# Optimization experiments

Measured on AMD Instinct MI355X. Metric: run time of the kernel, lower is better.

The kernel has to match this reference:

```python
import jax, jax.numpy as jnp
import numpy as np

B, N, F_IN, F_OUT, H = 2, 4096, 256, 64, 4


def setup_inputs() -> dict:
    key = jax.random.key(0)
    k_adj, k_h, k_w, k_l, k_r = jax.random.split(key, 5)
    adj = jax.random.randint(k_adj, (B, N, N), 0, 2, dtype=jnp.int32)
    h = jax.random.normal(k_h, (B, N, F_IN), dtype=jnp.float32)
    # xavier-uniform-ish params
    lim_w = float(np.sqrt(6.0 / (F_IN + F_OUT)))
    W = jax.random.uniform(k_w, (F_IN, F_OUT), jnp.float32, -lim_w, lim_w)
    lim_a = float(np.sqrt(6.0 / (F_OUT + H)))
    Wl = jax.random.uniform(k_l, (H, F_OUT), jnp.float32, -lim_a, lim_a)  # attn_l.weight
    Wr = jax.random.uniform(k_r, (H, F_OUT), jnp.float32, -lim_a, lim_a)  # attn_r.weight
    b = jnp.zeros((F_OUT,), jnp.float32)
    return {"adj": adj, "h": h, "W": W, "Wl": Wl, "Wr": Wr, "b": b}


def reference(adj, h, W, Wl, Wr, b):
    # dropout layers are identity in eval mode
    x = jnp.einsum('bnf,fo->bno', h, W)                       # (B,N,F_OUT)
    el = jnp.einsum('bno,ho->bnh', x, Wl)                     # (B,N,H)
    er = jnp.einsum('bno,ho->bnh', x, Wr)                     # (B,N,H)
    attn = el[:, :, None, :] + er[:, None, :, :]              # (B,N,N,H)
    attn = jax.nn.leaky_relu(attn, negative_slope=0.2)
    attn = jnp.where(adj[..., None] == 0, -jnp.inf, attn)
    attn = jax.nn.softmax(attn, axis=2)                       # softmax over source nodes j
    out = jnp.einsum('bijh,bjf->bihf', attn, x)               # (B,N,H,F_OUT)
    out = out + b                                             # bias over feature dim
    out = jax.nn.elu(out)                                     # activation
    return out.reshape(B, N, H * F_OUT)                       # n_heads>1 concat; B>1 keeps batch
```

## Files before the change

### kernel.cpp

```cpp
#include <hip/hip_runtime.h>
#include <hip/hip_bf16.h>


#define NN 4096
#define NH 4
#define JT 64
#define IT 64
#define NSET 4
#define NJQ 4
#define NTS ((NN / NJQ) / JT)
#define LOG2E 1.4426950408889634f

typedef __bf16 bf16x8 __attribute__((ext_vector_type(8)));
typedef unsigned short ushortx8 __attribute__((ext_vector_type(8)));
typedef unsigned short us4 __attribute__((ext_vector_type(4)));
typedef float f32x4 __attribute__((ext_vector_type(4)));

__device__ __forceinline__ void gload_lds16(const void* g, void* lds) {
  __builtin_amdgcn_global_load_lds(
      (const __attribute__((address_space(1))) void*)g,
      (__attribute__((address_space(3))) void*)lds, 16, 0, 0);
}

__device__ __forceinline__ unsigned short f2bf(float x) {
  __hip_bfloat16 hb = __float2bfloat16(x);
  return __builtin_bit_cast(unsigned short, hb);
}

#if __has_builtin(__builtin_amdgcn_exp2f)
#define EXP2F(x) __builtin_amdgcn_exp2f(x)
#else
#define EXP2F(x) exp2f(x)
#endif

__global__ __launch_bounds__(256, 2) void gat_prep(
    const float* __restrict__ hmat, const float* __restrict__ W,
    const float* __restrict__ Wl, const float* __restrict__ Wr,
    unsigned short* __restrict__ xT, float* __restrict__ elT,
    float* __restrict__ erT)
{
  __shared__ __align__(16) float h_s[16][256];
  __shared__ float x_s[16][65];
  __shared__ float wlr_s[512];

  const int t  = threadIdx.x;
  const int wv = t >> 6;
  const int l  = t & 63;
  const int b  = blockIdx.x >> 8;
  const int i0 = (blockIdx.x & 255) << 4;

  {
    const float4* hsrc = (const float4*)(hmat + ((size_t)(b * NN + i0)) * 256);
    float4* hdst = (float4*)&h_s[0][0];
#pragma unroll
    for (int u = 0; u < 4; ++u) hdst[t + 256 * u] = hsrc[t + 256 * u];
    wlr_s[t]       = Wl[t];
    wlr_s[256 + t] = Wr[t];
  }
  __syncthreads();

  const int row0 = wv << 2;
  float acc[4] = {0.f, 0.f, 0.f, 0.f};
#pragma unroll 4
  for (int k4 = 0; k4 < 64; ++k4) {
    const float w0 = W[(k4 * 4 + 0) * 64 + l];
    const float w1 = W[(k4 * 4 + 1) * 64 + l];
    const float w2 = W[(k4 * 4 + 2) * 64 + l];
    const float w3 = W[(k4 * 4 + 3) * 64 + l];
#pragma unroll
    for (int rr = 0; rr < 4; ++rr) {
      const float4 hv = *(const float4*)&h_s[row0 + rr][k4 * 4];
      acc[rr] = fmaf(hv.x, w0, acc[rr]);
      acc[rr] = fmaf(hv.y, w1, acc[rr]);
      acc[rr] = fmaf(hv.z, w2, acc[rr]);
      acc[rr] = fmaf(hv.w, w3, acc[rr]);
    }
  }
#pragma unroll
  for (int rr = 0; rr < 4; ++rr) x_s[row0 + rr][l] = acc[rr];
  __syncthreads();

  if (t < 64) {
    const int row = t >> 2, hh = t & 3;
    float el = 0.f, er = 0.f;
#pragma unroll 8
    for (int f = 0; f < 64; ++f) {
      const float xv = x_s[row][f];
      el = fmaf(xv, wlr_s[hh * 64 + f], el);
      er = fmaf(xv, wlr_s[256 + hh * 64 + f], er);
    }
    elT[((size_t)b * NH + hh) * NN + i0 + row] = el * LOG2E;
    erT[((size_t)b * NH + hh) * NN + i0 + row] = er * LOG2E;
  }

  {
    const int f = t >> 2, q = t & 3;
    us4 pk;
#pragma unroll
    for (int rj = 0; rj < 4; ++rj) pk[rj] = f2bf(x_s[q * 4 + rj][f]);
    *(us4*)&xT[((size_t)(b * 64 + f)) * NN + i0 + q * 4] = pk;
  }
}

template <bool ATOMIC>
__global__ __launch_bounds__(256, 2) void gat_main(
    const int* __restrict__ adj, const unsigned short* __restrict__ xT,
    const float* __restrict__ elT, const float* __restrict__ erT,
    float* __restrict__ numP, float* __restrict__ denP)
{
  __shared__ __align__(16) int            adj_lds[3][IT * JT];
  __shared__ __align__(16) unsigned short xt_lds[3][64 * JT];
  __shared__ __align__(16) float          er_lds[3][NH * JT];

  const int t = threadIdx.x;
  const int w = t >> 6;
  const int l = t & 63;
  const int b     = blockIdx.x >> 8;
  const int itile = (blockIdx.x & 255) >> 2;
  const int jq    = blockIdx.x & 3;
  const int i0    = itile << 6;
  const int j0b   = jq << 10;

  const int lrow = l & 15;
  const int lk   = l >> 4;

  float el_reg[NSET];
#pragma unroll
  for (int set = 0; set < NSET; ++set)
    el_reg[set] = elT[((size_t)b * NH + w) * NN + i0 + (set << 4) + lrow];

  auto issue_tile = [&](int j0, int s) {
#pragma unroll
    for (int g = 0; g < 4; ++g) {
      const int gi = (w << 2) + g;
      const int r  = (gi << 2) + (l >> 4);
      gload_lds16(adj + ((size_t)(b * NN + i0 + r)) * NN + j0 +
                      ((((l & 15) ^ (r & 7))) << 2),
                  &adj_lds[s][gi << 8]);
    }
#pragma unroll
    for (int g = 0; g < 2; ++g) {
      const int gi = (w << 1) + g;
      const int f  = (gi << 3) + (l >> 3);
      gload_lds16(xT + ((size_t)(b * 64 + f)) * NN + j0 +
                      ((((l & 7) ^ (f & 7))) << 3),
                  &xt_lds[s][gi << 9]);
    }
    if (w == 3) {
      const int h2 = l >> 4;
      gload_lds16(erT + ((size_t)b * NH + h2) * NN + j0 + ((l & 15) << 2),
                  &er_lds[s][0]);
    }
  };

  f32x4 acc[NSET][4] = {};
  f32x4 accd[NSET] = {};
  ushortx8 ones_u;
#pragma unroll
  for (int i = 0; i < 8; ++i) ones_u[i] = 0x3F80;
  const bf16x8 onesf = __builtin_bit_cast(bf16x8, ones_u);

  issue_tile(j0b, 0);
  issue_tile(j0b + JT, 1);

  for (int it = 0; it < NTS; ++it) {
    const int s = it % 3;
    if (it == NTS - 1) asm volatile("s_waitcnt vmcnt(0)" ::: "memory");
    else if (w < 3)    asm volatile("s_waitcnt vmcnt(6)" ::: "memory");
    else               asm volatile("s_waitcnt vmcnt(7)" ::: "memory");
    __builtin_amdgcn_s_barrier();
    __builtin_amdgcn_sched_barrier(0);

    if (it + 2 < NTS) issue_tile(j0b + (it + 2) * JT, (it + 2) % 3);

    float4 er_f[2][2];
    bf16x8 Axt[2][4];
#pragma unroll
    for (int kc = 0; kc < 2; ++kc) {
      er_f[kc][0] = *(const float4*)&er_lds[s][(w << 6) + (kc << 5) + (lk << 3)];
      er_f[kc][1] = *(const float4*)&er_lds[s][(w << 6) + (kc << 5) + (lk << 3) + 4];
#pragma unroll
      for (int fq = 0; fq < 4; ++fq) {
        const int f = (fq << 4) + lrow;
        const int c = ((kc << 2) + lk) ^ (f & 7);
        Axt[kc][fq] = __builtin_bit_cast(
            bf16x8, *(const ushortx8*)&xt_lds[s][(f << 6) + (c << 3)]);
      }
    }

#pragma unroll
    for (int set = 0; set < NSET; ++set) {
      const int r  = (set << 4) + lrow;
      const int rb = r << 6;
      const int sw = r & 7;
#pragma unroll
      for (int kc = 0; kc < 2; ++kc) {
        const int cb = (kc << 3) + (lk << 1);
        const int4 aj0 = *(const int4*)&adj_lds[s][rb + ((cb ^ sw) << 2)];
        const int4 aj1 = *(const int4*)&adj_lds[s][rb + (((cb + 1) ^ sw) << 2)];
        const float4 er0 = er_f[kc][0];
        const float4 er1 = er_f[kc][1];

        ushortx8 pa;
#define SCORE(A_, E_, IDX) { \
        float s_  = el_reg[set] + (E_); \
        float lr_ = fmaxf(s_, 0.2f * s_); \
        float w_  = (A_) ? EXP2F(lr_) : 0.0f; \
        pa[IDX] = f2bf(w_); }
        SCORE(aj0.x, er0.x, 0) SCORE(aj0.y, er0.y, 1)
        SCORE(aj0.z, er0.z, 2) SCORE(aj0.w, er0.w, 3)
        SCORE(aj1.x, er1.x, 4) SCORE(aj1.y, er1.y, 5)
        SCORE(aj1.z, er1.z, 6) SCORE(aj1.w, er1.w, 7)
#undef SCORE

        const bf16x8 P = __builtin_bit_cast(bf16x8, pa);
        accd[set] = __builtin_amdgcn_mfma_f32_16x16x32_bf16(onesf, P, accd[set], 0, 0, 0);
#pragma unroll
        for (int fq = 0; fq < 4; ++fq)
          acc[set][fq] = __builtin_amdgcn_mfma_f32_16x16x32_bf16(
              Axt[kc][fq], P, acc[set][fq], 0, 0, 0);
      }
    }
  }

  if (ATOMIC) {
#pragma unroll
    for (int set = 0; set < NSET; ++set) {
      const size_t obase = ((size_t)(b * NN + i0 + (set << 4) + lrow) * NH + w) << 6;
#pragma unroll
      for (int fq = 0; fq < 4; ++fq)
#pragma unroll
        for (int rr = 0; rr < 4; ++rr)
          atomicAdd(&numP[obase + (fq << 4) + (lk << 2) + rr], acc[set][fq][rr]);
    }
    if (l < 16) {
#pragma unroll
      for (int set = 0; set < NSET; ++set)
        atomicAdd(&denP[((size_t)(b * NN + i0 + (set << 4) + l)) * NH + w],
                  accd[set][0]);
    }
  } else {
    float* nb = numP + (size_t)jq * (2u * NN * NH * 64);
#pragma unroll
    for (int set = 0; set < NSET; ++set) {
      const size_t obase = ((size_t)(b * NN + i0 + (set << 4) + lrow) * NH + w) << 6;
#pragma unroll
      for (int fq = 0; fq < 4; ++fq)
        *(float4*)&nb[obase + (fq << 4) + (lk << 2)] = (float4){
            acc[set][fq][0], acc[set][fq][1], acc[set][fq][2], acc[set][fq][3]};
    }
    if (l < 16) {
      float* db = denP + (size_t)jq * (2u * NN * NH);
#pragma unroll
      for (int set = 0; set < NSET; ++set)
        db[((size_t)(b * NN + i0 + (set << 4) + l)) * NH + w] = accd[set][0];
    }
  }
}

template <bool ATOMIC>
__global__ __launch_bounds__(256) void gat_fin(
    const float* __restrict__ numP, const float* __restrict__ denP,
    const float* __restrict__ bias, float* __restrict__ out)
{
  const int g  = blockIdx.x * 256 + threadIdx.x;
  const int f4 = (g & 15) << 2;
  float4 n;
  float d;
  if (ATOMIC) {
    n = *(const float4*)&out[(size_t)g * 4];
    d = denP[g >> 4];
  } else {
    n = (float4){0.f, 0.f, 0.f, 0.f};
    d = 0.f;
#pragma unroll
    for (int q = 0; q < NJQ; ++q) {
      const float4 nq = *(const float4*)&numP[(size_t)q * (2u * NN * NH * 64) + (size_t)g * 4];
      n.x += nq.x; n.y += nq.y; n.z += nq.z; n.w += nq.w;
      d += denP[(size_t)q * (2u * NN * NH) + (g >> 4)];
    }
  }
  const float inv = 1.0f / d;
  const float4 bv = *(const float4*)&bias[f4];
  float4 v = {n.x * inv + bv.x, n.y * inv + bv.y,
              n.z * inv + bv.z, n.w * inv + bv.w};
  v.x = v.x > 0.f ? v.x : (__expf(v.x) - 1.f);
  v.y = v.y > 0.f ? v.y : (__expf(v.y) - 1.f);
  v.z = v.z > 0.f ? v.z : (__expf(v.z) - 1.f);
  v.w = v.w > 0.f ? v.w : (__expf(v.w) - 1.f);
  *(float4*)&out[(size_t)g * 4] = v;
}

extern "C" void kernel_launch(void* const* d_in, const int* in_sizes, int n_in,
                              void* d_out, int out_size, void* d_ws, size_t ws_size,
                              hipStream_t stream) {
  const int*   adj  = (const int*)d_in[0];
  const float* hmat = (const float*)d_in[1];
  const float* W    = (const float*)d_in[2];
  const float* Wl   = (const float*)d_in[3];
  const float* Wr   = (const float*)d_in[4];
  const float* bias = (const float*)d_in[5];
  float* out = (float*)d_out;

  char* wsb = (char*)d_ws;
  unsigned short* xT = (unsigned short*)wsb;
  float* elT = (float*)(wsb + 1048576);
  float* erT = (float*)(wsb + 1179648);
  float* den = (float*)(wsb + 1310720);
  float* num = (float*)(wsb + 1835008);
  const bool partial = ws_size >= 35389440ull;

  gat_prep<<<512, 256, 0, stream>>>(hmat, W, Wl, Wr, xT, elT, erT);

  if (partial) {
    gat_main<false><<<512, 256, 0, stream>>>(adj, xT, elT, erT, num, den);
    gat_fin<false><<<2048, 256, 0, stream>>>(num, den, bias, out);
  } else {
    hipMemsetAsync(out, 0, (size_t)out_size * 4, stream);
    hipMemsetAsync(den, 0, 131072, stream);
    gat_main<true><<<512, 256, 0, stream>>>(adj, xT, elT, erT, out, den);
    gat_fin<true><<<2048, 256, 0, stream>>>(num, den, bias, out);
  }
}
```

Measured before the change: 251.3 us.

## Pack adjacency into bitmasks in a pre-pass and consume bits in main kernel

```diff
diff --git a/kernel.cpp b/kernel.cpp
--- a/kernel.cpp
+++ b/kernel.cpp
@@ -5,10 +5,10 @@
 #define NN 4096
 #define NH 4
 #define JT 64
-#define IT 64
 #define NSET 4
 #define NJQ 4
-#define NTS ((NN / NJQ) / JT)
+#define JQW (NN / NJQ)
+#define NTS (JQW / JT)
 #define LOG2E 1.4426950408889634f
 
 typedef __bf16 bf16x8 __attribute__((ext_vector_type(8)));
@@ -32,6 +32,21 @@
 #else
 #define EXP2F(x) exp2f(x)
 #endif
+
+__global__ __launch_bounds__(256) void gat_pack(
+    const int* __restrict__ adj, unsigned long long* __restrict__ adjp)
+{
+  const int w = threadIdx.x >> 6, l = threadIdx.x & 63;
+  const int row = blockIdx.x * 4 + w;
+  const int* src = adj + (size_t)row * NN;
+  unsigned long long* dst = adjp + (size_t)row * 64;
+#pragma unroll 4
+  for (int it = 0; it < 64; ++it) {
+    const int v = src[it * 64 + l];
+    const unsigned long long m = __ballot(v != 0);
+    if (l == 0) dst[it] = m;
+  }
+}
 
 __global__ __launch_bounds__(256, 2) void gat_prep(
     const float* __restrict__ hmat, const float* __restrict__ W,
@@ -104,13 +119,14 @@
 
 template <bool ATOMIC>
 __global__ __launch_bounds__(256, 2) void gat_main(
-    const int* __restrict__ adj, const unsigned short* __restrict__ xT,
+    const unsigned long long* __restrict__ adjp,
+    const unsigned short* __restrict__ xT,
     const float* __restrict__ elT, const float* __restrict__ erT,
     float* __restrict__ numP, float* __restrict__ denP)
 {
-  __shared__ __align__(16) int            adj_lds[3][IT * JT];
+  __shared__ __align__(16) unsigned long long padj[64 * 16];
   __shared__ __align__(16) unsigned short xt_lds[3][64 * JT];
-  __shared__ __align__(16) float          er_lds[3][NH * JT];
+  __shared__ __align__(16) float er_lds[3][NH * JT];
 
   const int t = threadIdx.x;
   const int w = t >> 6;
@@ -129,15 +145,17 @@
   for (int set = 0; set < NSET; ++set)
     el_reg[set] = elT[((size_t)b * NH + w) * NN + i0 + (set << 4) + lrow];
 
+#pragma unroll
+  for (int g = 0; g < 2; ++g) {
+    const int gi  = (w << 1) + g;
+    const int row = (gi << 3) + (l >> 3);
+    const int c   = (l & 7) ^ (row & 7);
+    gload_lds16((const char*)adjp + ((size_t)(b * NN + i0 + row)) * 512 +
+                    (jq << 7) + (c << 4),
+                (char*)padj + (gi << 10));
+  }
+
   auto issue_tile = [&](int j0, int s) {
-#pragma unroll
-    for (int g = 0; g < 4; ++g) {
-      const int gi = (w << 2) + g;
-      const int r  = (gi << 2) + (l >> 4);
-      gload_lds16(adj + ((size_t)(b * NN + i0 + r)) * NN + j0 +
-                      ((((l & 15) ^ (r & 7))) << 2),
-                  &adj_lds[s][gi << 8]);
-    }
 #pragma unroll
     for (int g = 0; g < 2; ++g) {
       const int gi = (w << 1) + g;
@@ -166,8 +184,8 @@
   for (int it = 0; it < NTS; ++it) {
     const int s = it % 3;
     if (it == NTS - 1) asm volatile("s_waitcnt vmcnt(0)" ::: "memory");
-    else if (w < 3)    asm volatile("s_waitcnt vmcnt(6)" ::: "memory");
-    else               asm volatile("s_waitcnt vmcnt(7)" ::: "memory");
+    else if (w < 3)    asm volatile("s_waitcnt vmcnt(2)" ::: "memory");
+    else               asm volatile("s_waitcnt vmcnt(3)" ::: "memory");
     __builtin_amdgcn_s_barrier();
     __builtin_amdgcn_sched_barrier(0);
 
@@ -190,27 +208,28 @@
 
 #pragma unroll
     for (int set = 0; set < NSET; ++set) {
-      const int r  = (set << 4) + lrow;
-      const int rb = r << 6;
-      const int sw = r & 7;
+      const int r = (set << 4) + lrow;
+      const int cs = (it >> 1) ^ (r & 7);
+      const unsigned long long a = padj[(r << 4) + (cs << 1) + (it & 1)];
+      const unsigned byte0 = (unsigned)(a >> (lk << 3)) & 0xffu;
+      const unsigned byte1 = (unsigned)(a >> ((lk << 3) + 32)) & 0xffu;
+
 #pragma unroll
       for (int kc = 0; kc < 2; ++kc) {
-        const int cb = (kc << 3) + (lk << 1);
-        const int4 aj0 = *(const int4*)&adj_lds[s][rb + ((cb ^ sw) << 2)];
-        const int4 aj1 = *(const int4*)&adj_lds[s][rb + (((cb + 1) ^ sw) << 2)];
+        const unsigned by = kc ? byte1 : byte0;
         const float4 er0 = er_f[kc][0];
         const float4 er1 = er_f[kc][1];
 
         ushortx8 pa;
-#define SCORE(A_, E_, IDX) { \
+#define SCORE(BIT_, E_, IDX) { \
         float s_  = el_reg[set] + (E_); \
         float lr_ = fmaxf(s_, 0.2f * s_); \
-        float w_  = (A_) ? EXP2F(lr_) : 0.0f; \
+        float w_  = (by & (BIT_)) ? EXP2F(lr_) : 0.0f; \
         pa[IDX] = f2bf(w_); }
-        SCORE(aj0.x, er0.x, 0) SCORE(aj0.y, er0.y, 1)
-        SCORE(aj0.z, er0.z, 2) SCORE(aj0.w, er0.w, 3)
-        SCORE(aj1.x, er1.x, 4) SCORE(aj1.y, er1.y, 5)
-        SCORE(aj1.z, er1.z, 6) SCORE(aj1.w, er1.w, 7)
+        SCORE(1u,   er0.x, 0) SCORE(2u,   er0.y, 1)
+        SCORE(4u,   er0.z, 2) SCORE(8u,   er0.w, 3)
+        SCORE(16u,  er1.x, 4) SCORE(32u,  er1.y, 5)
+        SCORE(64u,  er1.z, 6) SCORE(128u, er1.w, 7)
 #undef SCORE
 
         const bf16x8 P = __builtin_bit_cast(bf16x8, pa);
@@ -303,22 +322,24 @@
   float* out = (float*)d_out;
 
   char* wsb = (char*)d_ws;
-  unsigned short* xT = (unsigned short*)wsb;
-  float* elT = (float*)(wsb + 1048576);
-  float* erT = (float*)(wsb + 1179648);
-  float* den = (float*)(wsb + 1310720);
-  float* num = (float*)(wsb + 1835008);
-  const bool partial = ws_size >= 35389440ull;
-
+  unsigned short*     xT   = (unsigned short*)wsb;
+  float*              elT  = (float*)(wsb + 1048576);
+  float*              erT  = (float*)(wsb + 1179648);
+  float*              den  = (float*)(wsb + 1310720);
+  unsigned long long* adjp = (unsigned long long*)(wsb + 1835008);
+  float*              num  = (float*)(wsb + 6029312);
+  const bool partial = ws_size >= 39583744ull;
+
+  gat_pack<<<2048, 256, 0, stream>>>(adj, adjp);
   gat_prep<<<512, 256, 0, stream>>>(hmat, W, Wl, Wr, xT, elT, erT);
 
   if (partial) {
-    gat_main<false><<<512, 256, 0, stream>>>(adj, xT, elT, erT, num, den);
+    gat_main<false><<<512, 256, 0, stream>>>(adjp, xT, elT, erT, num, den);
     gat_fin<false><<<2048, 256, 0, stream>>>(num, den, bias, out);
   } else {
     hipMemsetAsync(out, 0, (size_t)out_size * 4, stream);
     hipMemsetAsync(den, 0, 131072, stream);
-    gat_main<true><<<512, 256, 0, stream>>>(adj, xT, elT, erT, out, den);
+    gat_main<true><<<512, 256, 0, stream>>>(adjp, xT, elT, erT, out, den);
     gat_fin<true><<<2048, 256, 0, stream>>>(num, den, bias, out);
   }
 }
```

After: 294.4 us. 1.17x slower.

## Replace LDS-staged triple buffering with direct global loads and smaller row tiles

Applied to the files above, without the earlier changes.

```diff
diff --git a/kernel.cpp b/kernel.cpp
--- a/kernel.cpp
+++ b/kernel.cpp
@@ -4,23 +4,14 @@
 
 #define NN 4096
 #define NH 4
-#define JT 64
-#define IT 64
-#define NSET 4
-#define NJQ 4
-#define NTS ((NN / NJQ) / JT)
+#define NJQ 2
+#define NT 32
 #define LOG2E 1.4426950408889634f
 
 typedef __bf16 bf16x8 __attribute__((ext_vector_type(8)));
 typedef unsigned short ushortx8 __attribute__((ext_vector_type(8)));
 typedef unsigned short us4 __attribute__((ext_vector_type(4)));
 typedef float f32x4 __attribute__((ext_vector_type(4)));
-
-__device__ __forceinline__ void gload_lds16(const void* g, void* lds) {
-  __builtin_amdgcn_global_load_lds(
-      (const __attribute__((address_space(1))) void*)g,
-      (__attribute__((address_space(3))) void*)lds, 16, 0, 0);
-}
 
 __device__ __forceinline__ unsigned short f2bf(float x) {
   __hip_bfloat16 hb = __float2bfloat16(x);
@@ -103,157 +94,122 @@
 }
 
 template <bool ATOMIC>
-__global__ __launch_bounds__(256, 2) void gat_main(
+__global__ __launch_bounds__(256, 3) void gat_main(
     const int* __restrict__ adj, const unsigned short* __restrict__ xT,
     const float* __restrict__ elT, const float* __restrict__ erT,
     float* __restrict__ numP, float* __restrict__ denP)
 {
-  __shared__ __align__(16) int            adj_lds[3][IT * JT];
-  __shared__ __align__(16) unsigned short xt_lds[3][64 * JT];
-  __shared__ __align__(16) float          er_lds[3][NH * JT];
-
   const int t = threadIdx.x;
   const int w = t >> 6;
   const int l = t & 63;
-  const int b     = blockIdx.x >> 8;
-  const int itile = (blockIdx.x & 255) >> 2;
-  const int jq    = blockIdx.x & 3;
-  const int i0    = itile << 6;
-  const int j0b   = jq << 10;
-
+  const int blk   = blockIdx.x;
+  const int jh    = blk >> 9;
+  const int b     = (blk >> 8) & 1;
+  const int itile = blk & 255;
+  const int i0 = itile << 4;
+  const int j0 = jh << 11;
   const int lrow = l & 15;
   const int lk   = l >> 4;
 
-  float el_reg[NSET];
-#pragma unroll
-  for (int set = 0; set < NSET; ++set)
-    el_reg[set] = elT[((size_t)b * NH + w) * NN + i0 + (set << 4) + lrow];
-
-  auto issue_tile = [&](int j0, int s) {
-#pragma unroll
-    for (int g = 0; g < 4; ++g) {
-      const int gi = (w << 2) + g;
-      const int r  = (gi << 2) + (l >> 4);
-      gload_lds16(adj + ((size_t)(b * NN + i0 + r)) * NN + j0 +
-                      ((((l & 15) ^ (r & 7))) << 2),
-                  &adj_lds[s][gi << 8]);
-    }
-#pragma unroll
-    for (int g = 0; g < 2; ++g) {
-      const int gi = (w << 1) + g;
-      const int f  = (gi << 3) + (l >> 3);
-      gload_lds16(xT + ((size_t)(b * 64 + f)) * NN + j0 +
-                      ((((l & 7) ^ (f & 7))) << 3),
-                  &xt_lds[s][gi << 9]);
-    }
-    if (w == 3) {
-      const int h2 = l >> 4;
-      gload_lds16(erT + ((size_t)b * NH + h2) * NN + j0 + ((l & 15) << 2),
-                  &er_lds[s][0]);
-    }
-  };
-
-  f32x4 acc[NSET][4] = {};
-  f32x4 accd[NSET] = {};
+  const float el_reg = elT[((size_t)b * NH + w) * NN + i0 + lrow];
+
+  const int*            adjp = adj + ((size_t)(b * NN + i0 + lrow)) * NN + j0 + (lk << 3);
+  const unsigned short* xtp  = xT + (size_t)b * 64 * NN + j0 + (lk << 3);
+  const float*          erp  = erT + ((size_t)b * NH + w) * NN + j0 + (lk << 3);
+
+  f32x4 acc[4] = {};
+  f32x4 accd = {};
   ushortx8 ones_u;
 #pragma unroll
   for (int i = 0; i < 8; ++i) ones_u[i] = 0x3F80;
   const bf16x8 onesf = __builtin_bit_cast(bf16x8, ones_u);
 
-  issue_tile(j0b, 0);
-  issue_tile(j0b + JT, 1);
-
-  for (int it = 0; it < NTS; ++it) {
-    const int s = it % 3;
-    if (it == NTS - 1) asm volatile("s_waitcnt vmcnt(0)" ::: "memory");
-    else if (w < 3)    asm volatile("s_waitcnt vmcnt(6)" ::: "memory");
-    else               asm volatile("s_waitcnt vmcnt(7)" ::: "memory");
-    __builtin_amdgcn_s_barrier();
-    __builtin_amdgcn_sched_barrier(0);
-
-    if (it + 2 < NTS) issue_tile(j0b + (it + 2) * JT, (it + 2) % 3);
-
-    float4 er_f[2][2];
+  int4   a0 = *(const int4*)(adjp + 0);
+  int4   a1 = *(const int4*)(adjp + 4);
+  int4   a2 = *(const int4*)(adjp + 32);
+  int4   a3 = *(const int4*)(adjp + 36);
+  float4 e0 = *(const float4*)(erp + 0);
+  float4 e1 = *(const float4*)(erp + 4);
+  float4 e2 = *(const float4*)(erp + 32);
+  float4 e3 = *(const float4*)(erp + 36);
+
+#pragma unroll 1
+  for (int tt = 0; tt < NT; ++tt) {
+    const int jt = tt << 6;
+
     bf16x8 Axt[2][4];
 #pragma unroll
+    for (int kc = 0; kc < 2; ++kc)
+#pragma unroll
+      for (int fq = 0; fq < 4; ++fq)
+        Axt[kc][fq] = __builtin_bit_cast(bf16x8,
+            *(const ushortx8*)(xtp + (size_t)((fq << 4) + lrow) * NN + jt + (kc << 5)));
+
+    int4 n0 = a0, n1 = a1, n2 = a2, n3 = a3;
+    float4 f0 = e0, f1 = e1, f2 = e2, f3 = e3;
+    if (tt + 1 < NT) {
+      const int*   nb = adjp + jt + 64;
+      const float* fb = erp + jt + 64;
+      n0 = *(const int4*)(nb + 0);
+      n1 = *(const int4*)(nb + 4);
+      n2 = *(const int4*)(nb + 32);
+      n3 = *(const int4*)(nb + 36);
+      f0 = *(const float4*)(fb + 0);
+      f1 = *(const float4*)(fb + 4);
+      f2 = *(const float4*)(fb + 32);
+      f3 = *(const float4*)(fb + 36);
+    }
+
+#pragma unroll
     for (int kc = 0; kc < 2; ++kc) {
-      er_f[kc][0] = *(const float4*)&er_lds[s][(w << 6) + (kc << 5) + (lk << 3)];
-      er_f[kc][1] = *(const float4*)&er_lds[s][(w << 6) + (kc << 5) + (lk << 3) + 4];
-#pragma unroll
-      for (int fq = 0; fq < 4; ++fq) {
-        const int f = (fq << 4) + lrow;
-        const int c = ((kc << 2) + lk) ^ (f & 7);
-        Axt[kc][fq] = __builtin_bit_cast(
-            bf16x8, *(const ushortx8*)&xt_lds[s][(f << 6) + (c << 3)]);
-      }
-    }
-
-#pragma unroll
-    for (int set = 0; set < NSET; ++set) {
-      const int r  = (set << 4) + lrow;
-      const int rb = r << 6;
-      const int sw = r & 7;
-#pragma unroll
-      for (int kc = 0; kc < 2; ++kc) {
-        const int cb = (kc << 3) + (lk << 1);
-        const int4 aj0 = *(const int4*)&adj_lds[s][rb + ((cb ^ sw) << 2)];
-        const int4 aj1 = *(const int4*)&adj_lds[s][rb + (((cb + 1) ^ sw) << 2)];
-        const float4 er0 = er_f[kc][0];
-        const float4 er1 = er_f[kc][1];
-
-        ushortx8 pa;
+      const int4   ja = kc ? a2 : a0;
+      const int4   jb = kc ? a3 : a1;
+      const float4 ea = kc ? e2 : e0;
+      const float4 eb = kc ? e3 : e1;
+
+      ushortx8 pa;
 #define SCORE(A_, E_, IDX) { \
-        float s_  = el_reg[set] + (E_); \
-        float lr_ = fmaxf(s_, 0.2f * s_); \
-        float w_  = (A_) ? EXP2F(lr_) : 0.0f; \
-        pa[IDX] = f2bf(w_); }
-        SCORE(aj0.x, er0.x, 0) SCORE(aj0.y, er0.y, 1)
-        SCORE(aj0.z, er0.z, 2) SCORE(aj0.w, er0.w, 3)
-        SCORE(aj1.x, er1.x, 4) SCORE(aj1.y, er1.y, 5)
-        SCORE(aj1.z, er1.z, 6) SCORE(aj1.w, er1.w, 7)
+      float s_  = el_reg + (E_); \
+      float lr_ = fmaxf(s_, 0.2f * s_); \
+      float w_  = (A_) ? EXP2F(lr_) : 0.0f; \
+      pa[IDX] = f2bf(w_); }
+      SCORE(ja.x, ea.x, 0) SCORE(ja.y, ea.y, 1)
+      SCORE(ja.z, ea.z, 2) SCORE(ja.w, ea.w, 3)
+      SCORE(jb.x, eb.x, 4) SCORE(jb.y, eb.y, 5)
+      SCORE(jb.z, eb.z, 6) SCORE(jb.w, eb.w, 7)
 #undef SCORE
 
-        const bf16x8 P = __builtin_bit_cast(bf16x8, pa);
-        accd[set] = __builtin_amdgcn_mfma_f32_16x16x32_bf16(onesf, P, accd[set], 0, 0, 0);
-#pragma unroll
-        for (int fq = 0; fq < 4; ++fq)
-          acc[set][fq] = __builtin_amdgcn_mfma_f32_16x16x32_bf16(
-              Axt[kc][fq], P, acc[set][fq], 0, 0, 0);
-      }
-    }
+      const bf16x8 P = __builtin_bit_cast(bf16x8, pa);
+      accd = __builtin_amdgcn_mfma_f32_16x16x32_bf16(onesf, P, accd, 0, 0, 0);
+#pragma unroll
+      for (int fq = 0; fq < 4; ++fq)
+        acc[fq] = __builtin_amdgcn_mfma_f32_16x16x32_bf16(
+            Axt[kc][fq], P, acc[fq], 0, 0, 0);
+    }
+
+    a0 = n0; a1 = n1; a2 = n2; a3 = n3;
+    e0 = f0; e1 = f1; e2 = f2; e3 = f3;
   }
 
   if (ATOMIC) {
-#pragma unroll
-    for (int set = 0; set < NSET; ++set) {
-      const size_t obase = ((size_t)(b * NN + i0 + (set << 4) + lrow) * NH + w) << 6;
-#pragma unroll
-      for (int fq = 0; fq < 4; ++fq)
-#pragma unroll
-        for (int rr = 0; rr < 4; ++rr)
-          atomicAdd(&numP[obase + (fq << 4) + (lk << 2) + rr], acc[set][fq][rr]);
-    }
+    const size_t obase = ((size_t)(b * NN + i0 + lrow) * NH + w) << 6;
+#pragma unroll
+    for (int fq = 0; fq < 4; ++fq)
+#pragma unroll
+      for (int rr = 0; rr < 4; ++rr)
+        atomicAdd(&numP[obase + (fq << 4) + (lk << 2) + rr], acc[fq][rr]);
+    if (l < 16)
+      atomicAdd(&denP[((size_t)(b * NN + i0 + l)) * NH + w], accd[0]);
+  } else {
+    float* nb = numP + (size_t)jh * (2u * NN * NH * 64);
+    const size_t obase = ((size_t)(b * NN + i0 + lrow) * NH + w) << 6;
+#pragma unroll
+    for (int fq = 0; fq < 4; ++fq)
+      *(float4*)&nb[obase + (fq << 4) + (lk << 2)] = (float4){
+          acc[fq][0], acc[fq][1], acc[fq][2], acc[fq][3]};
     if (l < 16) {
-#pragma unroll
-      for (int set = 0; set < NSET; ++set)
-        atomicAdd(&denP[((size_t)(b * NN + i0 + (set << 4) + l)) * NH + w],
-                  accd[set][0]);
-    }
-  } else {
-    float* nb = numP + (size_t)jq * (2u * NN * NH * 64);
-#pragma unroll
-    for (int set = 0; set < NSET; ++set) {
-      const size_t obase = ((size_t)(b * NN + i0 + (set << 4) + lrow) * NH + w) << 6;
-#pragma unroll
-      for (int fq = 0; fq < 4; ++fq)
-        *(float4*)&nb[obase + (fq << 4) + (lk << 2)] = (float4){
-            acc[set][fq][0], acc[set][fq][1], acc[set][fq][2], acc[set][fq][3]};
-    }
-    if (l < 16) {
-      float* db = denP + (size_t)jq * (2u * NN * NH);
-#pragma unroll
-      for (int set = 0; set < NSET; ++set)
-        db[((size_t)(b * NN + i0 + (set << 4) + l)) * NH + w] = accd[set][0];
+      float* db = denP + (size_t)jh * (2u * NN * NH);
+      db[((size_t)(b * NN + i0 + l)) * NH + w] = accd[0];
     }
   }
 }
@@ -303,22 +259,22 @@
   float* out = (float*)d_out;
 
   char* wsb = (char*)d_ws;
-  unsigned short* xT = (unsigned short*)wsb;
-  float* elT = (float*)(wsb + 1048576);
-  float* erT = (float*)(wsb + 1179648);
-  float* den = (float*)(wsb + 1310720);
-  float* num = (float*)(wsb + 1835008);
-  const bool partial = ws_size >= 35389440ull;
+  unsigned short* xT  = (unsigned short*)wsb;
+  float*          elT = (float*)(wsb + 1048576);
+  float*          erT = (float*)(wsb + 1179648);
+  float*          den = (float*)(wsb + 1310720);
+  float*          num = (float*)(wsb + 1572864);
+  const bool partial = ws_size >= 18350080ull;
 
   gat_prep<<<512, 256, 0, stream>>>(hmat, W, Wl, Wr, xT, elT, erT);
 
   if (partial) {
-    gat_main<false><<<512, 256, 0, stream>>>(adj, xT, elT, erT, num, den);
+    gat_main<false><<<1024, 256, 0, stream>>>(adj, xT, elT, erT, num, den);
     gat_fin<false><<<2048, 256, 0, stream>>>(num, den, bias, out);
   } else {
     hipMemsetAsync(out, 0, (size_t)out_size * 4, stream);
     hipMemsetAsync(den, 0, 131072, stream);
-    gat_main<true><<<512, 256, 0, stream>>>(adj, xT, elT, erT, out, den);
+    gat_main<true><<<1024, 256, 0, stream>>>(adj, xT, elT, erT, out, den);
     gat_fin<true><<<2048, 256, 0, stream>>>(num, den, bias, out);
   }
 }
```

Result: slower. 361.3 us (+43.8%).
